# Kernel optimization log

Hardware: AMD Instinct MI355X
Metric: run time of the kernel (lower is better)

## Reference

```python
import jax, jax.numpy as jnp
import numpy as np

N = 50000        # nodes
E = 800000       # edges (avg degree 16)
F = 64           # in/out feature dim (scatter into zeros_like(x) forces out==in)
H = 128          # hidden dim
CIN = 2 * F + 1  # combined_features dim


def setup_inputs() -> dict:
    key = jax.random.key(0)
    ks = jax.random.split(key, 12)
    x = jax.random.normal(ks[0], (N, F), dtype=jnp.float32)
    pos = jax.random.normal(ks[1], (N, 3), dtype=jnp.float32)
    edge_index = jax.random.randint(ks[2], (2, E), 0, N, dtype=jnp.int64)
    s1 = 1.0 / np.sqrt(CIN)
    s2 = 1.0 / np.sqrt(H)
    W1x = jax.random.uniform(ks[3], (CIN, H), jnp.float32, -s1, s1)
    b1x = jax.random.uniform(ks[4], (H,), jnp.float32, -s1, s1)
    W2x = jax.random.uniform(ks[5], (H, F), jnp.float32, -s2, s2)
    b2x = jax.random.uniform(ks[6], (F,), jnp.float32, -s2, s2)
    W1p = jax.random.uniform(ks[7], (CIN, H), jnp.float32, -s1, s1)
    b1p = jax.random.uniform(ks[8], (H,), jnp.float32, -s1, s1)
    W2p = jax.random.uniform(ks[9], (H, 1), jnp.float32, -s2, s2)
    b2p = jax.random.uniform(ks[10], (1,), jnp.float32, -s2, s2)
    return {"x": x, "pos": pos, "edge_index": edge_index,
            "W1x": W1x, "b1x": b1x, "W2x": W2x, "b2x": b2x,
            "W1p": W1p, "b1p": b1p, "W2p": W2p, "b2p": b2p}


def reference(x, pos, edge_index, W1x, b1x, W2x, b2x, W1p, b1p, W2p, b2p):
    row, col = edge_index[0], edge_index[1]
    rel_pos = pos[row] - pos[col]                              # [E, 3]
    dist_sq = jnp.sum(rel_pos * rel_pos, axis=-1, keepdims=True)  # [E, 1]
    combined = jnp.concatenate([x[row], x[col], dist_sq], axis=-1)  # [E, 2F+1]
    # phi_x: Linear -> SiLU -> Linear
    msg_x = jax.nn.silu(combined @ W1x + b1x) @ W2x + b2x      # [E, F]
    aggregated_x = jax.ops.segment_sum(msg_x, col, num_segments=x.shape[0])
    # phi_pos: Linear -> SiLU -> Linear (scalar weight per edge)
    weight_pos = jax.nn.silu(combined @ W1p + b1p) @ W2p + b2p  # [E, 1]
    pos_update = weight_pos * rel_pos                           # [E, 3]
    aggregated_pos = jax.ops.segment_sum(pos_update, col, num_segments=pos.shape[0])
    return aggregated_x, aggregated_pos
```

## Files before the change

kernel.cpp:

```cpp
#include <hip/hip_runtime.h>

typedef short short8 __attribute__((ext_vector_type(8)));
typedef float floatx4 __attribute__((ext_vector_type(4)));

__device__ __forceinline__ unsigned short f2bf(float f) {
  unsigned int u = __float_as_uint(f);
  u += 0x7FFFu + ((u >> 16) & 1u);
  return (unsigned short)(u >> 16);
}

#if __has_builtin(__builtin_amdgcn_cvt_pk_bf16_f32)
typedef __bf16 bf16x2_t __attribute__((ext_vector_type(2)));
__device__ __forceinline__ unsigned int pk2bf(float lo, float hi) {
  bf16x2_t v = __builtin_amdgcn_cvt_pk_bf16_f32(lo, hi);
  return __builtin_bit_cast(unsigned int, v);
}
#else
__device__ __forceinline__ unsigned int pk2bf(float lo, float hi) {
  return (unsigned)f2bf(lo) | ((unsigned)f2bf(hi) << 16);
}
#endif

__device__ __forceinline__ float silu(float h) {
  return h * __builtin_amdgcn_rcpf(1.f + __expf(-h));
}

__global__ __launch_bounds__(256) void k_mega(
    float* __restrict__ out, int out_n,
    const int* __restrict__ colp, int E, int* __restrict__ hist,
    const float* __restrict__ x, int N,
    const float* __restrict__ W1x, const float* __restrict__ W1p,
    const float* __restrict__ W2x,
    const float* __restrict__ b1x, const float* __restrict__ b1p,
    unsigned short* __restrict__ wbuf,
    unsigned int* __restrict__ Ar, unsigned int* __restrict__ Ac,
    int b1, int b2, int b3)
{
  __shared__ __align__(16) unsigned short xt[64][72];
  const int blk = blockIdx.x, t = threadIdx.x;

  if (blk < b1) {
    const int n0 = blk * 64;
    const int wv = t >> 6, lane = t & 63, quad = lane >> 4, lc = lane & 15;

    {
      int nd = t >> 2, p = t & 3;
      int n = n0 + nd;
      uint4 o0, o1;
      if (n < N) {
        const float4* xp = (const float4*)(x + (size_t)n*64 + p*16);
        float4 a = xp[0], b = xp[1], c = xp[2], d = xp[3];
        o0 = make_uint4(pk2bf(a.x,a.y), pk2bf(a.z,a.w), pk2bf(b.x,b.y), pk2bf(b.z,b.w));
        o1 = make_uint4(pk2bf(c.x,c.y), pk2bf(c.z,c.w), pk2bf(d.x,d.y), pk2bf(d.z,d.w));
      } else {
        o0 = o1 = make_uint4(0u,0u,0u,0u);
      }
      *(uint4*)&xt[nd][p*16]     = o0;
      *(uint4*)&xt[nd][p*16 + 8] = o1;
    }

    short8 fxr[2][2], fxc[2][2], fpr[2][2], fpc[2][2];
    float bxv[2][4], bpv[2][4];
    #pragma unroll
    for (int ti = 0; ti < 2; ++ti) {
      const int nt = wv + 4*ti;
      const int n  = nt*16 + lc;
      #pragma unroll
      for (int k2 = 0; k2 < 2; ++k2) {
        #pragma unroll
        for (int j = 0; j < 8; ++j) {
          const int kr = k2*32 + quad*8 + j;
          fxr[ti][k2][j] = (short)f2bf(W1x[kr*128 + n]);
          fxc[ti][k2][j] = (short)f2bf(W1x[(64 + kr)*128 + n]);
          fpr[ti][k2][j] = (short)f2bf(W1p[kr*128 + n]);
          fpc[ti][k2][j] = (short)f2bf(W1p[(64 + kr)*128 + n]);
        }
      }
      #pragma unroll
      for (int r = 0; r < 4; ++r) {
        bxv[ti][r] = b1x[nt*16 + quad*4 + r];
        bpv[ti][r] = b1p[nt*16 + quad*4 + r];
      }
    }
    __syncthreads();

    #pragma unroll 1
    for (int mw = 0; mw < 4; ++mw) {
      short8 bb0 = *(const short8*)&xt[mw*16 + lc][quad*8];
      short8 bb1 = *(const short8*)&xt[mw*16 + lc][32 + quad*8];
      const int nd = n0 + mw*16 + lc;
      #pragma unroll
      for (int ti = 0; ti < 2; ++ti) {
        floatx4 xr = {0,0,0,0}, xc = {0,0,0,0}, pr = {0,0,0,0}, pc = {0,0,0,0};
        xr = __builtin_amdgcn_mfma_f32_16x16x32_bf16(fxr[ti][0], bb0, xr, 0,0,0);
        xr = __builtin_amdgcn_mfma_f32_16x16x32_bf16(fxr[ti][1], bb1, xr, 0,0,0);
        xc = __builtin_amdgcn_mfma_f32_16x16x32_bf16(fxc[ti][0], bb0, xc, 0,0,0);
        xc = __builtin_amdgcn_mfma_f32_16x16x32_bf16(fxc[ti][1], bb1, xc, 0,0,0);
        pr = __builtin_amdgcn_mfma_f32_16x16x32_bf16(fpr[ti][0], bb0, pr, 0,0,0);
        pr = __builtin_amdgcn_mfma_f32_16x16x32_bf16(fpr[ti][1], bb1, pr, 0,0,0);
        pc = __builtin_amdgcn_mfma_f32_16x16x32_bf16(fpc[ti][0], bb0, pc, 0,0,0);
        pc = __builtin_amdgcn_mfma_f32_16x16x32_bf16(fpc[ti][1], bb1, pc, 0,0,0);
        if (nd < N) {
          const int hbase = (wv + 4*ti)*16 + quad*4;
          uint4 ur = make_uint4(pk2bf(xr[0]+bxv[ti][0], pr[0]+bpv[ti][0]),
                                pk2bf(xr[1]+bxv[ti][1], pr[1]+bpv[ti][1]),
                                pk2bf(xr[2]+bxv[ti][2], pr[2]+bpv[ti][2]),
                                pk2bf(xr[3]+bxv[ti][3], pr[3]+bpv[ti][3]));
          uint4 uc = make_uint4(pk2bf(xc[0], pc[0]), pk2bf(xc[1], pc[1]),
                                pk2bf(xc[2], pc[2]), pk2bf(xc[3], pc[3]));
          *(uint4*)(Ar + (size_t)nd*128 + hbase) = ur;
          *(uint4*)(Ac + (size_t)nd*128 + hbase) = uc;
        }
      }
    }
  } else if (blk < b2) {
    int i = ((blk - b1) * 256 + t) * 16;
    #pragma unroll
    for (int q = 0; q < 4; ++q) {
      int j = i + q*4;
      if (j + 4 <= out_n) *(float4*)(out + j) = make_float4(0.f,0.f,0.f,0.f);
      else for (int k = j; k < out_n; ++k) out[k] = 0.f;
    }
  } else if (blk < b3) {
    int i4 = (blk - b2) * 256 + t;
    if (i4 < (E >> 2)) {
      int4 c = *(const int4*)(colp + i4*4);
      atomicAdd(&hist[c.x], 1); atomicAdd(&hist[c.y], 1);
      atomicAdd(&hist[c.z], 1); atomicAdd(&hist[c.w], 1);
    }
    if (blk == b2 && t == 0)
      for (int k = E & ~3; k < E; ++k) atomicAdd(&hist[colp[k]], 1);
  } else {
    int i = (blk - b3) * 256 + t;
    if (i < 8192) {
      int jj = i & 7, lane = (i >> 3) & 63, ks = (i >> 9) & 3, nt = (i >> 11) & 3;
      int k = ks*32 + (lane >> 4)*8 + jj;
      wbuf[i] = f2bf(W2x[k*64 + nt*16 + (lane & 15)]);
    }
  }
}

__global__ __launch_bounds__(256) void k_scan_a(
    int* __restrict__ hist, int N, int* __restrict__ bsum) {
  __shared__ int wtot[4], wexc[4];
  int t = threadIdx.x, lane = t & 63, w = t >> 6;
  int base = blockIdx.x * 1024 + t * 4;
  int v0 = (base + 0 < N) ? hist[base + 0] : 0;
  int v1 = (base + 1 < N) ? hist[base + 1] : 0;
  int v2 = (base + 2 < N) ? hist[base + 2] : 0;
  int v3 = (base + 3 < N) ? hist[base + 3] : 0;
  int T = v0 + v1 + v2 + v3;
  int inc = T;
  #pragma unroll
  for (int s = 1; s < 64; s <<= 1) {
    int u = __shfl_up(inc, s, 64);
    if (lane >= s) inc += u;
  }
  if (lane == 63) wtot[w] = inc;
  __syncthreads();
  if (t == 0) {
    int a = 0;
    #pragma unroll
    for (int i = 0; i < 4; ++i) { wexc[i] = a; a += wtot[i]; }
    bsum[blockIdx.x] = a;
  }
  __syncthreads();
  int tex = wexc[w] + (inc - T);
  if (base + 0 < N) hist[base + 0] = tex;
  if (base + 1 < N) hist[base + 1] = tex + v0;
  if (base + 2 < N) hist[base + 2] = tex + v0 + v1;
  if (base + 3 < N) hist[base + 3] = tex + v0 + v1 + v2;
}

__global__ __launch_bounds__(256) void k_scatter(
    const int* __restrict__ row, const int* __restrict__ col, int E,
    int* __restrict__ excl, const int* __restrict__ bsum, int NB,
    int2* __restrict__ sedge) {
  __shared__ int boff_sh[64];
  int t = threadIdx.x;
  if (t < 64) {
    int v = (t < NB) ? bsum[t] : 0;
    int inc = v;
    #pragma unroll
    for (int s = 1; s < 64; s <<= 1) {
      int u = __shfl_up(inc, s, 64);
      if (t >= s) inc += u;
    }
    boff_sh[t] = inc - v;
  }
  __syncthreads();
  int i4 = blockIdx.x * 256 + t;
  if (i4 < (E >> 2)) {
    int4 c = *(const int4*)(col + i4*4);
    int4 r = *(const int4*)(row + i4*4);
    int p;
    p = atomicAdd(&excl[c.x], 1) + boff_sh[c.x >> 10]; sedge[p] = make_int2(r.x, c.x);
    p = atomicAdd(&excl[c.y], 1) + boff_sh[c.y >> 10]; sedge[p] = make_int2(r.y, c.y);
    p = atomicAdd(&excl[c.z], 1) + boff_sh[c.z >> 10]; sedge[p] = make_int2(r.z, c.z);
    p = atomicAdd(&excl[c.w], 1) + boff_sh[c.w >> 10]; sedge[p] = make_int2(r.w, c.w);
  }
  if (blockIdx.x == 0 && t == 0) {
    for (int k = E & ~3; k < E; ++k) {
      int c = col[k];
      int p = atomicAdd(&excl[c], 1) + boff_sh[c >> 10];
      sedge[p] = make_int2(row[k], c);
    }
  }
}

__global__ __launch_bounds__(256) void mp_main(
    const float* __restrict__ pos,
    const int2* __restrict__ sedge, int E,
    const unsigned int* __restrict__ Ar, const unsigned int* __restrict__ Ac,
    const float* __restrict__ W1x, const float* __restrict__ W1p,
    const float* __restrict__ b2x, const float* __restrict__ W2p,
    const float* __restrict__ b2p,
    const unsigned short* __restrict__ wbuf,
    float* __restrict__ out_x, float* __restrict__ out_pos)
{
  __shared__ __align__(16) unsigned short H_lds[64][136];
  __shared__ __align__(16) uint4 edata[64];
  __shared__ float rel_lds[64][3];
  __shared__ int   col_sh[64];
  __shared__ float wsum[4][64];

  const int t    = threadIdx.x;
  const int e0   = blockIdx.x * 64;
  const int wv   = t >> 6;
  const int lane = t & 63;
  const int quad = lane >> 4;
  const int lc   = lane & 15;

  if (t < 64) {
    int e = e0 + t;
    int r = 0, c = 0, cs = -1;
    float rp0 = 0.f, rp1 = 0.f, rp2 = 0.f, dsq = 0.f;
    if (e < E) {
      int2 rc = sedge[e]; r = rc.x; c = rc.y;
      cs = c;
      float pr0 = pos[r*3+0], pr1 = pos[r*3+1], pr2 = pos[r*3+2];
      float pc0 = pos[c*3+0], pc1 = pos[c*3+1], pc2 = pos[c*3+2];
      rp0 = pr0 - pc0; rp1 = pr1 - pc1; rp2 = pr2 - pc2;
      dsq = rp0*rp0 + rp1*rp1 + rp2*rp2;
    }
    rel_lds[t][0] = rp0; rel_lds[t][1] = rp1; rel_lds[t][2] = rp2;
    col_sh[t] = cs;
    edata[t] = make_uint4((unsigned)r, (unsigned)c, __float_as_uint(dsq), 0u);
  }

  const short8* __restrict__ w2x_f = (const short8*)wbuf;
  short8 a2w[4];
  #pragma unroll
  for (int ks = 0; ks < 4; ++ks) a2w[ks] = w2x_f[(wv*4 + ks)*64 + lane];

  float w1xd[2][4], w1pd[2][4], wp2[2][4], b2xr[4];
  #pragma unroll
  for (int ti = 0; ti < 2; ++ti)
    #pragma unroll
    for (int r = 0; r < 4; ++r) {
      int h = (wv + 4*ti)*16 + quad*4 + r;
      w1xd[ti][r] = W1x[16384 + h];
      w1pd[ti][r] = W1p[16384 + h];
      wp2[ti][r]  = W2p[h];
    }
  #pragma unroll
  for (int r = 0; r < 4; ++r) b2xr[r] = b2x[wv*16 + quad*4 + r];
  const float b2ps = b2p[0];
  __syncthreads();

  #pragma unroll
  for (int et = 0; et < 4; ++et) {
    uint4 ed = edata[et*16 + lc];
    const float dsqv = __uint_as_float(ed.z);
    float ps = 0.f;
    #pragma unroll
    for (int ti = 0; ti < 2; ++ti) {
      const int ht = wv + 4*ti;
      const int hb = ht*32 + quad*8;
      uint4 va = *(const uint4*)((const unsigned short*)Ar + (size_t)ed.x*256 + hb);
      uint4 vc = *(const uint4*)((const unsigned short*)Ac + (size_t)ed.y*256 + hb);
      float sx[4];
      #pragma unroll
      for (int j = 0; j < 4; ++j) {
        unsigned a = (&va.x)[j], bb = (&vc.x)[j];
        float hx = __uint_as_float(a << 16) + __uint_as_float(bb << 16)
                 + dsqv * w1xd[ti][j];
        float hp = __uint_as_float(a & 0xffff0000u) + __uint_as_float(bb & 0xffff0000u)
                 + dsqv * w1pd[ti][j];
        sx[j] = silu(hx);
        ps += silu(hp) * wp2[ti][j];
      }
      *(uint2*)&H_lds[et*16 + lc][ht*16 + quad*4] =
          make_uint2(pk2bf(sx[0], sx[1]), pk2bf(sx[2], sx[3]));
    }
    ps += __shfl_xor(ps, 16, 64);
    ps += __shfl_xor(ps, 32, 64);
    if (lane < 16) wsum[wv][et*16 + lane] = ps;
  }
  __syncthreads();

  #pragma unroll 2
  for (int et = 0; et < 4; ++et) {
    floatx4 acc = {0,0,0,0};
    #pragma unroll
    for (int ks = 0; ks < 4; ++ks) {
      short8 b = *(const short8*)&H_lds[et*16 + lc][ks*32 + quad*8];
      acc = __builtin_amdgcn_mfma_f32_16x16x32_bf16(a2w[ks], b, acc, 0, 0, 0);
    }
    int edge = et*16 + lc;
    int myc = col_sh[edge];
    float v0 = acc[0] + b2xr[0], v1 = acc[1] + b2xr[1];
    float v2 = acc[2] + b2xr[2], v3 = acc[3] + b2xr[3];
    #pragma unroll
    for (int s = 1; s < 16; s <<= 1) {
      int   nc = __shfl_down(myc, s, 64);
      float n0 = __shfl_down(v0,  s, 64);
      float n1 = __shfl_down(v1,  s, 64);
      float n2 = __shfl_down(v2,  s, 64);
      float n3 = __shfl_down(v3,  s, 64);
      if ((lc + s < 16) && (nc == myc)) { v0 += n0; v1 += n1; v2 += n2; v3 += n3; }
    }
    bool head = (myc >= 0) && (lc == 0 || col_sh[edge-1] != myc);
    if (head) {
      float* dst = out_x + (size_t)myc*64 + wv*16 + quad*4;
      atomicAdd(dst + 0, v0);
      atomicAdd(dst + 1, v1);
      atomicAdd(dst + 2, v2);
      atomicAdd(dst + 3, v3);
    }
  }

  if (t < 64) {
    int c = col_sh[t];
    float w = wsum[0][t] + wsum[1][t] + wsum[2][t] + wsum[3][t] + b2ps;
    float p0 = w * rel_lds[t][0], p1 = w * rel_lds[t][1], p2 = w * rel_lds[t][2];
    #pragma unroll
    for (int s = 1; s < 64; s <<= 1) {
      int   nc = __shfl_down(c,  s, 64);
      float n0 = __shfl_down(p0, s, 64);
      float n1 = __shfl_down(p1, s, 64);
      float n2 = __shfl_down(p2, s, 64);
      if ((t + s < 64) && (nc == c)) { p0 += n0; p1 += n1; p2 += n2; }
    }
    bool head = (c >= 0) && (t == 0 || col_sh[t-1] != c);
    if (head) {
      atomicAdd(&out_pos[(size_t)c*3 + 0], p0);
      atomicAdd(&out_pos[(size_t)c*3 + 1], p1);
      atomicAdd(&out_pos[(size_t)c*3 + 2], p2);
    }
  }
}

extern "C" void kernel_launch(void* const* d_in, const int* in_sizes, int n_in,
                              void* d_out, int out_size, void* d_ws, size_t ws_size,
                              hipStream_t stream) {
  const float* x   = (const float*)d_in[0];
  const float* pos = (const float*)d_in[1];
  const int*   ei  = (const int*)d_in[2];
  const float* W1x = (const float*)d_in[3];
  const float* b1x = (const float*)d_in[4];
  const float* W2x = (const float*)d_in[5];
  const float* b2x = (const float*)d_in[6];
  const float* W1p = (const float*)d_in[7];
  const float* b1p = (const float*)d_in[8];
  const float* W2p = (const float*)d_in[9];
  const float* b2p = (const float*)d_in[10];

  const int E = in_sizes[2] / 2;
  const int N = in_sizes[0] / 64;
  const int* rowp = ei;
  const int* colp = ei + E;
  float* out_x   = (float*)d_out;
  float* out_pos = out_x + (size_t)N * 64;
  const int NB = (N + 1023) / 1024;

  char* ws = (char*)d_ws;
  const size_t tab_one = (size_t)N * 512;
  unsigned int*   Ar   = (unsigned int*)ws;
  unsigned int*   Ac   = (unsigned int*)(ws + tab_one);
  unsigned short* wbuf = (unsigned short*)(ws + 2*tab_one);
  int*  hist  = (int*)(ws + 2*tab_one + 16384);
  int*  bsum  = (int*)(ws + 2*tab_one + 16384 + 200192);
  int2* sedge = (int2*)(ws + 2*tab_one + 16384 + 200192 + 512);

  hipMemsetAsync(hist, 0, (size_t)N * sizeof(int), stream);

  const int nb_node = (N + 63) / 64;
  const int nb_zero = (out_size + 4095) / 4096;
  const int nb_hist = ((E >> 2) + 255) / 256;
  const int nb_rep  = 32;
  const int b1 = nb_node, b2 = b1 + nb_zero, b3 = b2 + nb_hist;
  k_mega<<<b3 + nb_rep, 256, 0, stream>>>(
      (float*)d_out, out_size, colp, E, hist, x, N,
      W1x, W1p, W2x, b1x, b1p, wbuf, Ar, Ac, b1, b2, b3);

  k_scan_a<<<NB, 256, 0, stream>>>(hist, N, bsum);
  k_scatter<<<((E >> 2) + 255) / 256, 256, 0, stream>>>(
      rowp, colp, E, hist, bsum, NB, sedge);

  mp_main<<<(E + 63) / 64, 256, 0, stream>>>(
      pos, sedge, E, Ar, Ac, W1x, W1p, b2x, W2p, b2p, wbuf, out_x, out_pos);
}
```

Baseline: 312.0 us.

## Rebalance setup kernels: move node precompute into the edge scatter launch

Splits the former mega setup kernel so that zeroing, the histogram and the W2 repack run first. The per-node Ar/Ac MFMA precompute now shares a launch with the edge counting-sort scatter after the scan. The launch count stays the same, but the light histogram kernel no longer waits behind the heavy node GEMM, and the node work overlaps the atomic-bound scatter. This adds a shared-memory allocation and a barrier to the scatter branch and changes which block ranges run together.

```diff
diff --git a/kernel.cpp b/kernel.cpp
--- a/kernel.cpp
+++ b/kernel.cpp
@@ -25,16 +25,80 @@
   return h * __builtin_amdgcn_rcpf(1.f + __expf(-h));
 }
 
-__global__ __launch_bounds__(256) void k_mega(
+__global__ __launch_bounds__(256) void k_setup1(
     float* __restrict__ out, int out_n,
     const int* __restrict__ colp, int E, int* __restrict__ hist,
+    const float* __restrict__ W2x, unsigned short* __restrict__ wbuf,
+    int b1, int b2)
+{
+  const int blk = blockIdx.x, t = threadIdx.x;
+  if (blk < b1) {
+    int i = (blk * 256 + t) * 16;
+    #pragma unroll
+    for (int q = 0; q < 4; ++q) {
+      int j = i + q*4;
+      if (j + 4 <= out_n) *(float4*)(out + j) = make_float4(0.f,0.f,0.f,0.f);
+      else for (int k = j; k < out_n; ++k) out[k] = 0.f;
+    }
+  } else if (blk < b2) {
+    int i4 = (blk - b1) * 256 + t;
+    if (i4 < (E >> 2)) {
+      int4 c = *(const int4*)(colp + i4*4);
+      atomicAdd(&hist[c.x], 1); atomicAdd(&hist[c.y], 1);
+      atomicAdd(&hist[c.z], 1); atomicAdd(&hist[c.w], 1);
+    }
+    if (blk == b1 && t == 0)
+      for (int k = E & ~3; k < E; ++k) atomicAdd(&hist[colp[k]], 1);
+  } else {
+    int i = (blk - b2) * 256 + t;
+    if (i < 8192) {
+      int jj = i & 7, lane = (i >> 3) & 63, ks = (i >> 9) & 3, nt = (i >> 11) & 3;
+      int k = ks*32 + (lane >> 4)*8 + jj;
+      wbuf[i] = f2bf(W2x[k*64 + nt*16 + (lane & 15)]);
+    }
+  }
+}
+
+__global__ __launch_bounds__(256) void k_scan_a(
+    int* __restrict__ hist, int N, int* __restrict__ bsum) {
+  __shared__ int wtot[4], wexc[4];
+  int t = threadIdx.x, lane = t & 63, w = t >> 6;
+  int base = blockIdx.x * 1024 + t * 4;
+  int v0 = (base + 0 < N) ? hist[base + 0] : 0;
+  int v1 = (base + 1 < N) ? hist[base + 1] : 0;
+  int v2 = (base + 2 < N) ? hist[base + 2] : 0;
+  int v3 = (base + 3 < N) ? hist[base + 3] : 0;
+  int T = v0 + v1 + v2 + v3;
+  int inc = T;
+  #pragma unroll
+  for (int s = 1; s < 64; s <<= 1) {
+    int u = __shfl_up(inc, s, 64);
+    if (lane >= s) inc += u;
+  }
+  if (lane == 63) wtot[w] = inc;
+  __syncthreads();
+  if (t == 0) {
+    int a = 0;
+    #pragma unroll
+    for (int i = 0; i < 4; ++i) { wexc[i] = a; a += wtot[i]; }
+    bsum[blockIdx.x] = a;
+  }
+  __syncthreads();
+  int tex = wexc[w] + (inc - T);
+  if (base + 0 < N) hist[base + 0] = tex;
+  if (base + 1 < N) hist[base + 1] = tex + v0;
+  if (base + 2 < N) hist[base + 2] = tex + v0 + v1;
+  if (base + 3 < N) hist[base + 3] = tex + v0 + v1 + v2;
+}
+
+__global__ __launch_bounds__(256) void k_setup2(
     const float* __restrict__ x, int N,
     const float* __restrict__ W1x, const float* __restrict__ W1p,
-    const float* __restrict__ W2x,
     const float* __restrict__ b1x, const float* __restrict__ b1p,
-    unsigned short* __restrict__ wbuf,
     unsigned int* __restrict__ Ar, unsigned int* __restrict__ Ac,
-    int b1, int b2, int b3)
+    const int* __restrict__ rowp, const int* __restrict__ colp, int E,
+    int* __restrict__ excl, const int* __restrict__ bsum, int NB,
+    int2* __restrict__ sedge, int b1)
 {
   __shared__ __align__(16) unsigned short xt[64][72];
   const int blk = blockIdx.x, t = threadIdx.x;
@@ -113,97 +177,35 @@
         }
       }
     }
-  } else if (blk < b2) {
-    int i = ((blk - b1) * 256 + t) * 16;
-    #pragma unroll
-    for (int q = 0; q < 4; ++q) {
-      int j = i + q*4;
-      if (j + 4 <= out_n) *(float4*)(out + j) = make_float4(0.f,0.f,0.f,0.f);
-      else for (int k = j; k < out_n; ++k) out[k] = 0.f;
-    }
-  } else if (blk < b3) {
-    int i4 = (blk - b2) * 256 + t;
+  } else {
+    __shared__ int boff_sh[64];
+    if (t < 64) {
+      int v = (t < NB) ? bsum[t] : 0;
+      int inc = v;
+      #pragma unroll
+      for (int s = 1; s < 64; s <<= 1) {
+        int u = __shfl_up(inc, s, 64);
+        if (t >= s) inc += u;
+      }
+      boff_sh[t] = inc - v;
+    }
+    __syncthreads();
+    int i4 = (blk - b1) * 256 + t;
     if (i4 < (E >> 2)) {
       int4 c = *(const int4*)(colp + i4*4);
-      atomicAdd(&hist[c.x], 1); atomicAdd(&hist[c.y], 1);
-      atomicAdd(&hist[c.z], 1); atomicAdd(&hist[c.w], 1);
-    }
-    if (blk == b2 && t == 0)
-      for (int k = E & ~3; k < E; ++k) atomicAdd(&hist[colp[k]], 1);
-  } else {
-    int i = (blk - b3) * 256 + t;
-    if (i < 8192) {
-      int jj = i & 7, lane = (i >> 3) & 63, ks = (i >> 9) & 3, nt = (i >> 11) & 3;
-      int k = ks*32 + (lane >> 4)*8 + jj;
-      wbuf[i] = f2bf(W2x[k*64 + nt*16 + (lane & 15)]);
-    }
-  }
-}
-
-__global__ __launch_bounds__(256) void k_scan_a(
-    int* __restrict__ hist, int N, int* __restrict__ bsum) {
-  __shared__ int wtot[4], wexc[4];
-  int t = threadIdx.x, lane = t & 63, w = t >> 6;
-  int base = blockIdx.x * 1024 + t * 4;
-  int v0 = (base + 0 < N) ? hist[base + 0] : 0;
-  int v1 = (base + 1 < N) ? hist[base + 1] : 0;
-  int v2 = (base + 2 < N) ? hist[base + 2] : 0;
-  int v3 = (base + 3 < N) ? hist[base + 3] : 0;
-  int T = v0 + v1 + v2 + v3;
-  int inc = T;
-  #pragma unroll
-  for (int s = 1; s < 64; s <<= 1) {
-    int u = __shfl_up(inc, s, 64);
-    if (lane >= s) inc += u;
-  }
-  if (lane == 63) wtot[w] = inc;
-  __syncthreads();
-  if (t == 0) {
-    int a = 0;
-    #pragma unroll
-    for (int i = 0; i < 4; ++i) { wexc[i] = a; a += wtot[i]; }
-    bsum[blockIdx.x] = a;
-  }
-  __syncthreads();
-  int tex = wexc[w] + (inc - T);
-  if (base + 0 < N) hist[base + 0] = tex;
-  if (base + 1 < N) hist[base + 1] = tex + v0;
-  if (base + 2 < N) hist[base + 2] = tex + v0 + v1;
-  if (base + 3 < N) hist[base + 3] = tex + v0 + v1 + v2;
-}
-
-__global__ __launch_bounds__(256) void k_scatter(
-    const int* __restrict__ row, const int* __restrict__ col, int E,
-    int* __restrict__ excl, const int* __restrict__ bsum, int NB,
-    int2* __restrict__ sedge) {
-  __shared__ int boff_sh[64];
-  int t = threadIdx.x;
-  if (t < 64) {
-    int v = (t < NB) ? bsum[t] : 0;
-    int inc = v;
-    #pragma unroll
-    for (int s = 1; s < 64; s <<= 1) {
-      int u = __shfl_up(inc, s, 64);
-      if (t >= s) inc += u;
-    }
-    boff_sh[t] = inc - v;
-  }
-  __syncthreads();
-  int i4 = blockIdx.x * 256 + t;
-  if (i4 < (E >> 2)) {
-    int4 c = *(const int4*)(col + i4*4);
-    int4 r = *(const int4*)(row + i4*4);
-    int p;
-    p = atomicAdd(&excl[c.x], 1) + boff_sh[c.x >> 10]; sedge[p] = make_int2(r.x, c.x);
-    p = atomicAdd(&excl[c.y], 1) + boff_sh[c.y >> 10]; sedge[p] = make_int2(r.y, c.y);
-    p = atomicAdd(&excl[c.z], 1) + boff_sh[c.z >> 10]; sedge[p] = make_int2(r.z, c.z);
-    p = atomicAdd(&excl[c.w], 1) + boff_sh[c.w >> 10]; sedge[p] = make_int2(r.w, c.w);
-  }
-  if (blockIdx.x == 0 && t == 0) {
-    for (int k = E & ~3; k < E; ++k) {
-      int c = col[k];
-      int p = atomicAdd(&excl[c], 1) + boff_sh[c >> 10];
-      sedge[p] = make_int2(row[k], c);
+      int4 r = *(const int4*)(rowp + i4*4);
+      int p;
+      p = atomicAdd(&excl[c.x], 1) + boff_sh[c.x >> 10]; sedge[p] = make_int2(r.x, c.x);
+      p = atomicAdd(&excl[c.y], 1) + boff_sh[c.y >> 10]; sedge[p] = make_int2(r.y, c.y);
+      p = atomicAdd(&excl[c.z], 1) + boff_sh[c.z >> 10]; sedge[p] = make_int2(r.z, c.z);
+      p = atomicAdd(&excl[c.w], 1) + boff_sh[c.w >> 10]; sedge[p] = make_int2(r.w, c.w);
+    }
+    if (blk == b1 && t == 0) {
+      for (int k = E & ~3; k < E; ++k) {
+        int c = colp[k];
+        int p = atomicAdd(&excl[c], 1) + boff_sh[c >> 10];
+        sedge[p] = make_int2(rowp[k], c);
+      }
     }
   }
 }
@@ -385,18 +387,20 @@
 
   hipMemsetAsync(hist, 0, (size_t)N * sizeof(int), stream);
 
-  const int nb_node = (N + 63) / 64;
   const int nb_zero = (out_size + 4095) / 4096;
   const int nb_hist = ((E >> 2) + 255) / 256;
   const int nb_rep  = 32;
-  const int b1 = nb_node, b2 = b1 + nb_zero, b3 = b2 + nb_hist;
-  k_mega<<<b3 + nb_rep, 256, 0, stream>>>(
-      (float*)d_out, out_size, colp, E, hist, x, N,
-      W1x, W1p, W2x, b1x, b1p, wbuf, Ar, Ac, b1, b2, b3);
+  const int s1b1 = nb_zero, s1b2 = s1b1 + nb_hist;
+  k_setup1<<<s1b2 + nb_rep, 256, 0, stream>>>(
+      (float*)d_out, out_size, colp, E, hist, W2x, wbuf, s1b1, s1b2);
 
   k_scan_a<<<NB, 256, 0, stream>>>(hist, N, bsum);
-  k_scatter<<<((E >> 2) + 255) / 256, 256, 0, stream>>>(
-      rowp, colp, E, hist, bsum, NB, sedge);
+
+  const int nb_node = (N + 63) / 64;
+  const int nb_scat = ((E >> 2) + 255) / 256;
+  k_setup2<<<nb_node + nb_scat, 256, 0, stream>>>(
+      x, N, W1x, W1p, b1x, b1p, Ar, Ac,
+      rowp, colp, E, hist, bsum, NB, sedge, nb_node);
 
   mp_main<<<(E + 63) / 64, 256, 0, stream>>>(
       pos, sedge, E, Ar, Ac, W1x, W1p, b2x, W2p, b2p, wbuf, out_x, out_pos);
```

Result: slower. 324.0 us (+3.9%).
